# Kernel optimization log

Hardware: AMD Instinct MI355X
Metric: run time of the kernel (lower is better)

Reference implementation:

```python
import math
import jax, jax.numpy as jnp
import numpy as np

B, T, C = 2, 2048, 2048
NQ, NKV, H = 16, 4, 128
EPS = 1e-6
ROPE_BASE = 5.0e6


def setup_inputs() -> dict:
    key = jax.random.key(0)
    ks = jax.random.split(key, 6)
    x = jax.random.normal(ks[0], (B, T, C), dtype=jnp.float32)
    s = 0.02
    Wq = jax.random.normal(ks[1], (C, NQ * H), dtype=jnp.float32) * s
    Wk = jax.random.normal(ks[2], (C, NKV * H), dtype=jnp.float32) * s
    Wv = jax.random.normal(ks[3], (C, NKV * H), dtype=jnp.float32) * s
    Wo = jax.random.normal(ks[4], (NQ * H, C), dtype=jnp.float32) * s
    q_norm_w = jnp.ones((H,), dtype=jnp.float32)
    k_norm_w = jnp.ones((H,), dtype=jnp.float32)
    # RoPE tables (seq_start = 0)
    inv_freq = 1.0 / (ROPE_BASE ** (jnp.arange(0, H, 2, dtype=jnp.float32) / H))
    t = jnp.arange(T, dtype=jnp.float32)
    freqs = jnp.einsum('i,j->ij', t, inv_freq)          # [T, H/2]
    emb = jnp.concatenate([freqs, freqs], axis=-1)       # [T, H]
    cos = jnp.cos(emb)
    sin = jnp.sin(emb)
    # additive causal mask (finite large negative to stay nan-free)
    causal = jnp.tril(jnp.ones((T, T), dtype=bool))
    attn_mask = jnp.where(causal, 0.0, -1e9).astype(jnp.float32)
    return {"x": x, "Wq": Wq, "Wk": Wk, "Wv": Wv, "Wo": Wo,
            "q_norm_w": q_norm_w, "k_norm_w": k_norm_w,
            "cos": cos, "sin": sin, "attn_mask": attn_mask}


def _rms_norm(x, w):
    # x: [..., H]
    var = jnp.mean(x * x, axis=-1, keepdims=True)
    return w * (x * jax.lax.rsqrt(var + EPS))


def _rotate_half(x):
    x1, x2 = jnp.split(x, 2, axis=-1)
    return jnp.concatenate([-x2, x1], axis=-1)


def reference(x, Wq, Wk, Wv, Wo, q_norm_w, k_norm_w, cos, sin, attn_mask):
    q = (x @ Wq).reshape(B, T, NQ, H)
    k = (x @ Wk).reshape(B, T, NKV, H)
    v = (x @ Wv).reshape(B, T, NKV, H)
    q = _rms_norm(q, q_norm_w)
    k = _rms_norm(k, k_norm_w)
    c = cos[None, :, None, :]  # [1,T,1,H]
    s = sin[None, :, None, :]
    q = q * c + _rotate_half(q) * s
    k = k * c + _rotate_half(k) * s
    rep = NQ // NKV
    k = jnp.repeat(k, rep, axis=2)  # [B,T,NQ,H]
    v = jnp.repeat(v, rep, axis=2)
    scores = jnp.einsum('bihd,bjhd->bhij', q, k) / math.sqrt(H)
    scores = scores + attn_mask[None, None, :, :]
    probs = jax.nn.softmax(scores, axis=-1)
    ctx = jnp.einsum('bhij,bjhd->bihd', probs, v).reshape(B, T, NQ * H)
    return ctx @ Wo
```

## Files before the change

kernel.cpp:

```cpp
#include <hip/hip_runtime.h>
#include <hip/hip_bf16.h>

#define B_   2
#define T_   2048
#define C_   2048
#define NQ_  16
#define NKV_ 4
#define H_   128

using bf16x8 = __attribute__((ext_vector_type(8))) short;
using f32x4  = __attribute__((ext_vector_type(4))) float;

__device__ __forceinline__ unsigned short f2bf(float f) {
    __hip_bfloat16 h = __float2bfloat16(f);
    union { __hip_bfloat16 h; unsigned short s; } c;
    c.h = h;
    return c.s;
}
__device__ __forceinline__ float bf2f(unsigned short s) {
    return __uint_as_float(((unsigned)s) << 16);
}
__device__ __forceinline__ bf16x8 pack8(float4 f0, float4 f1) {
    bf16x8 r;
    r[0] = (short)f2bf(f0.x); r[1] = (short)f2bf(f0.y);
    r[2] = (short)f2bf(f0.z); r[3] = (short)f2bf(f0.w);
    r[4] = (short)f2bf(f1.x); r[5] = (short)f2bf(f1.y);
    r[6] = (short)f2bf(f1.z); r[7] = (short)f2bf(f1.w);
    return r;
}

#define MFMA16(a, b, c) __builtin_amdgcn_mfma_f32_16x16x32_bf16(a, b, c, 0, 0, 0)

__global__ void transpose_cvt(const float* __restrict__ src,
                              unsigned short* __restrict__ dst,
                              int R, int Cc) {
    const int tc = Cc >> 6;
    const int r0 = (blockIdx.x / tc) * 64;
    const int c0 = (blockIdx.x % tc) * 64;
    __shared__ unsigned short Tl[64 * 65];
    const int tid = threadIdx.x;
#pragma unroll
    for (int it = 0; it < 16; ++it) {
        const int idx = it * 256 + tid;
        const int r = idx >> 6, c = idx & 63;
        Tl[c * 65 + r] = f2bf(src[(size_t)(r0 + r) * Cc + c0 + c]);
    }
    __syncthreads();
#pragma unroll
    for (int it = 0; it < 16; ++it) {
        const int idx = it * 256 + tid;
        const int c = idx >> 6, r = idx & 63;
        dst[(size_t)(c0 + c) * R + r0 + r] = Tl[c * 65 + r];
    }
}

#define LDP 40

template <bool A_BF, bool OUT_F32>
__global__ __launch_bounds__(256, 2) void gemm_bt(
    const void* __restrict__ Av,
    const unsigned short* __restrict__ Bt,
    void* __restrict__ Cqv,
    unsigned short* __restrict__ Ck,
    unsigned short* __restrict__ Cv,
    int M, int N, int K, int fused) {
    const int ntn = N >> 7;
    const int tm  = blockIdx.x / ntn;
    const int tn  = blockIdx.x % ntn;

    const int tid  = threadIdx.x;
    const int wv   = tid >> 6;
    const int lane = tid & 63;
    const int col  = lane & 15;
    const int quad = lane >> 4;
    const int wm   = (wv & 1) * 64;
    const int wn   = (wv >> 1) * 64;

    __shared__ unsigned short Al[128 * LDP];
    __shared__ unsigned short Bl[128 * LDP];

    f32x4 acc[4][4];
#pragma unroll
    for (int mt = 0; mt < 4; ++mt)
#pragma unroll
        for (int nt = 0; nt < 4; ++nt) acc[mt][nt] = (f32x4){0.f, 0.f, 0.f, 0.f};

    const int i1 = tid, i2 = tid + 256;
    const size_t aoff1 = (size_t)(tm * 128 + (i1 >> 2)) * K + (i1 & 3) * 8;
    const size_t aoff2 = (size_t)(tm * 128 + (i2 >> 2)) * K + (i2 & 3) * 8;
    const size_t boff1 = (size_t)(tn * 128 + (i1 >> 2)) * K + (i1 & 3) * 8;
    const size_t boff2 = (size_t)(tn * 128 + (i2 >> 2)) * K + (i2 & 3) * 8;
    unsigned short* Aw1 = Al + (i1 >> 2) * LDP + (i1 & 3) * 8;
    unsigned short* Aw2 = Al + (i2 >> 2) * LDP + (i2 & 3) * 8;
    unsigned short* Bw1 = Bl + (i1 >> 2) * LDP + (i1 & 3) * 8;
    unsigned short* Bw2 = Bl + (i2 >> 2) * LDP + (i2 & 3) * 8;

    const unsigned short* Ab16 = (const unsigned short*)Av;
    const float*          Af   = (const float*)Av;

    uint4  a1u, a2u, b1u, b2u;
    float4 a1lo, a1hi, a2lo, a2hi;

    auto loadAB = [&](int kk) {
        if constexpr (A_BF) {
            a1u = *(const uint4*)(Ab16 + aoff1 + kk);
            a2u = *(const uint4*)(Ab16 + aoff2 + kk);
        } else {
            a1lo = *(const float4*)(Af + aoff1 + kk);
            a1hi = *(const float4*)(Af + aoff1 + kk + 4);
            a2lo = *(const float4*)(Af + aoff2 + kk);
            a2hi = *(const float4*)(Af + aoff2 + kk + 4);
        }
        b1u = *(const uint4*)(Bt + boff1 + kk);
        b2u = *(const uint4*)(Bt + boff2 + kk);
    };

    loadAB(0);

    for (int k0 = 0; k0 < K; k0 += 32) {
        __syncthreads();
        if constexpr (A_BF) {
            *(uint4*)Aw1 = a1u;
            *(uint4*)Aw2 = a2u;
        } else {
            *(bf16x8*)Aw1 = pack8(a1lo, a1hi);
            *(bf16x8*)Aw2 = pack8(a2lo, a2hi);
        }
        *(uint4*)Bw1 = b1u;
        *(uint4*)Bw2 = b2u;
        __syncthreads();

        const int kn = (k0 + 32 < K) ? k0 + 32 : k0;
        loadAB(kn);

        bf16x8 af[4], bfv[4];
#pragma unroll
        for (int t = 0; t < 4; ++t) {
            af[t]  = *(const bf16x8*)(Al + (wm + t * 16 + col) * LDP + quad * 8);
            bfv[t] = *(const bf16x8*)(Bl + (wn + t * 16 + col) * LDP + quad * 8);
        }
#pragma unroll
        for (int mt = 0; mt < 4; ++mt)
#pragma unroll
            for (int nt = 0; nt < 4; ++nt)
                acc[mt][nt] = MFMA16(af[mt], bfv[nt], acc[mt][nt]);
    }

    const int nb = tn * 128;
    if constexpr (OUT_F32) {
        float* Co = (float*)Cqv;
#pragma unroll
        for (int mt = 0; mt < 4; ++mt)
#pragma unroll
            for (int nt = 0; nt < 4; ++nt)
#pragma unroll
                for (int r = 0; r < 4; ++r) {
                    const int row = tm * 128 + wm + mt * 16 + quad * 4 + r;
                    const int cc  = nb + wn + nt * 16 + col;
                    Co[(size_t)row * N + cc] = acc[mt][nt][r];
                }
    } else {
        unsigned short* Cb;
        int ldc, nc0;
        if (!fused)         { Cb = (unsigned short*)Cqv; ldc = N;    nc0 = nb;        }
        else if (nb < 2048) { Cb = (unsigned short*)Cqv; ldc = 2048; nc0 = nb;        }
        else if (nb < 2560) { Cb = Ck;                   ldc = 512;  nc0 = nb - 2048; }
        else                { Cb = Cv;                   ldc = 512;  nc0 = nb - 2560; }
#pragma unroll
        for (int mt = 0; mt < 4; ++mt)
#pragma unroll
            for (int nt = 0; nt < 4; ++nt)
#pragma unroll
                for (int r = 0; r < 4; ++r) {
                    const int row = tm * 128 + wm + mt * 16 + quad * 4 + r;
                    const int cc  = nc0 + wn + nt * 16 + col;
                    Cb[(size_t)row * ldc + cc] = f2bf(acc[mt][nt][r]);
                }
    }
}

__global__ void norm_rope(unsigned short* __restrict__ buf,
                          const float* __restrict__ w,
                          const float* __restrict__ cosb,
                          const float* __restrict__ sinb,
                          int nheads, float oscale) {
    const int idx = blockIdx.x;
    const int h   = idx % nheads;
    const int bt  = idx / nheads;
    const int t   = bt % T_;
    unsigned short* row = buf + ((size_t)bt * nheads + h) * H_;
    const int l = threadIdx.x;

    const float x0 = bf2f(row[l]);
    const float x1 = bf2f(row[l + 64]);
    float ss = x0 * x0 + x1 * x1;
#pragma unroll
    for (int off = 32; off; off >>= 1) ss += __shfl_xor(ss, off);
    const float r = rsqrtf(ss * (1.0f / 128.0f) + 1e-6f) * oscale;

    const float n0 = x0 * r * w[l];
    const float n1 = x1 * r * w[l + 64];
    const float c0 = cosb[t * H_ + l];
    const float c1 = cosb[t * H_ + l + 64];
    const float s0 = sinb[t * H_ + l];
    const float s1 = sinb[t * H_ + l + 64];

    row[l]      = f2bf(n0 * c0 - n1 * s0);
    row[l + 64] = f2bf(n1 * c1 + n0 * s1);
}

__global__ __launch_bounds__(512, 2) void flash_attn(
    const unsigned short* __restrict__ qbuf,
    const unsigned short* __restrict__ kbuf,
    const unsigned short* __restrict__ vbuf,
    unsigned short* __restrict__ ctx) {
    const int blk = blockIdx.x;
    const int p   = blk & 7;
    const int h   = (blk >> 3) & 15;
    const int b   = blk >> 7;
    const int kvh = h >> 2;
    const int qtB = 15 - p;

    const int tid  = threadIdx.x;
    const int wave = tid >> 6;
    const int g    = wave >> 2;
    const int gw   = wave & 3;
    const int lane = tid & 63;
    const int col  = lane & 15;
    const int quad = lane >> 4;
    const int gtid = gw * 64 + lane;

    int w0 = (g ? qtB : p) * 128 + gw * 32;
    const int ph1 = 2 * p + 2;

    __shared__ __align__(16) unsigned char smem[76800];
    unsigned short* Vg   = (unsigned short*)smem + g * 9216;
    unsigned short* Pw   = (unsigned short*)(smem + 36864) + wave * 2304;
    float*          alfw = (float*)(smem + 73728) + wave * 32;
    unsigned*       Vw   = (unsigned*)Vg;

    bf16x8 qf[2][4];
    auto loadQ = [&]() {
#pragma unroll
        for (int nt = 0; nt < 2; ++nt)
#pragma unroll
            for (int ks = 0; ks < 4; ++ks) {
                const size_t off =
                    ((size_t)(b * T_ + w0 + nt * 16 + col) * NQ_ + h) * H_ + ks * 32 + quad * 8;
                qf[nt][ks] = *(const bf16x8*)(qbuf + off);
            }
    };
    loadQ();

    f32x4 O[2][8];
#pragma unroll
    for (int pt = 0; pt < 2; ++pt)
#pragma unroll
        for (int dt = 0; dt < 8; ++dt) O[pt][dt] = (f32x4){0.f, 0.f, 0.f, 0.f};
    float m_run[2] = {-3.0e38f, -3.0e38f};
    float l_run[2] = {0.f, 0.f};

    bf16x8 kf[4][4];
    const unsigned short* kb = kbuf + ((size_t)(b * T_) * NKV_ + kvh) * H_;
    const int koff = col * (NKV_ * H_) + quad * 8;
    auto loadK = [&](int j0) {
#pragma unroll
        for (int mt = 0; mt < 4; ++mt) {
            const unsigned short* kr = kb + (size_t)((j0 + mt * 16) * (NKV_ * H_) + koff);
#pragma unroll
            for (int ks = 0; ks < 4; ++ks)
                kf[mt][ks] = *(const bf16x8*)(kr + ks * 32);
        }
    };

    uint4 va[4];
    const size_t kvstride = (size_t)NKV_ * H_;
    auto issueV = [&](int j0) {
#pragma unroll
        for (int it = 0; it < 2; ++it) {
            const int idx = it * 256 + gtid;
            const int kp  = idx & 31;
            const int dc  = idx >> 5;
            const size_t g0 = ((size_t)(b * T_ + j0 + 2 * kp) * NKV_ + kvh) * H_ + dc * 8;
            va[2 * it]     = *(const uint4*)(vbuf + g0);
            va[2 * it + 1] = *(const uint4*)(vbuf + g0 + kvstride);
        }
    };
    auto writeV = [&]() {
#pragma unroll
        for (int it = 0; it < 2; ++it) {
            const int idx = it * 256 + gtid;
            const int kp  = idx & 31;
            const int dc  = idx >> 5;
            const uint4 v0 = va[2 * it];
            const uint4 v1 = va[2 * it + 1];
            const int wb = dc * 288 + kp;
            Vw[wb + 0 * 36] = (v0.x & 0xFFFFu) | (v1.x << 16);
            Vw[wb + 1 * 36] = (v0.x >> 16)     | (v1.x & 0xFFFF0000u);
            Vw[wb + 2 * 36] = (v0.y & 0xFFFFu) | (v1.y << 16);
            Vw[wb + 3 * 36] = (v0.y >> 16)     | (v1.y & 0xFFFF0000u);
            Vw[wb + 4 * 36] = (v0.z & 0xFFFFu) | (v1.z << 16);
            Vw[wb + 5 * 36] = (v0.z >> 16)     | (v1.z & 0xFFFF0000u);
            Vw[wb + 6 * 36] = (v0.w & 0xFFFFu) | (v1.w << 16);
            Vw[wb + 7 * 36] = (v0.w >> 16)     | (v1.w & 0xFFFF0000u);
        }
    };

    auto storeOut = [&]() {
        if (quad == 0) {
            alfw[col]      = 1.0f / l_run[0];
            alfw[col + 16] = 1.0f / l_run[1];
        }
        const f32x4 i0 = *(const f32x4*)&alfw[quad * 4];
        const f32x4 i1 = *(const f32x4*)&alfw[quad * 4 + 16];
#pragma unroll
        for (int pt = 0; pt < 2; ++pt)
#pragma unroll
            for (int r = 0; r < 4; ++r) {
                const float inv = pt ? i1[r] : i0[r];
                const int ig = w0 + pt * 16 + quad * 4 + r;
                unsigned short* op = ctx + ((size_t)(b * T_ + ig) * NQ_ + h) * H_;
#pragma unroll
                for (int dt = 0; dt < 8; ++dt)
                    op[dt * 16 + col] = f2bf(O[pt][dt][r] * inv);
            }
    };

    auto chunk_of = [&](int i) { return g ? i : (i < ph1 ? i : i + 15 - 2 * p); };

    loadK(0);
    issueV(0);

    for (int i = 0; i < 17; ++i) {
        const int j0 = chunk_of(i) * 64;
        __syncthreads();
        writeV();
        __syncthreads();

        if (i + 1 < 17) issueV(chunk_of(i + 1) * 64);

        if (g == 0 && i == ph1) {
            storeOut();
#pragma unroll
            for (int pt = 0; pt < 2; ++pt)
#pragma unroll
                for (int dt = 0; dt < 8; ++dt) O[pt][dt] = (f32x4){0.f, 0.f, 0.f, 0.f};
            m_run[0] = m_run[1] = -3.0e38f;
            l_run[0] = l_run[1] = 0.f;
            w0 = qtB * 128 + gw * 32;
            loadQ();
        }

        const bool act = (j0 <= w0 + 31);

        f32x4 St[4][2];
        if (act) {
#pragma unroll
            for (int mt = 0; mt < 4; ++mt)
#pragma unroll
                for (int nt = 0; nt < 2; ++nt) St[mt][nt] = (f32x4){0.f, 0.f, 0.f, 0.f};
#pragma unroll
            for (int ks = 0; ks < 4; ++ks)
#pragma unroll
                for (int mt = 0; mt < 4; ++mt) {
                    St[mt][0] = MFMA16(kf[mt][ks], qf[0][ks], St[mt][0]);
                    St[mt][1] = MFMA16(kf[mt][ks], qf[1][ks], St[mt][1]);
                }
        }

        if (i + 1 < 17) loadK(chunk_of(i + 1) * 64);

        if (!act) continue;

        const bool needmask = (j0 + 63 > w0);
        if (needmask) {
            const int ig0 = w0 + col;
#pragma unroll
            for (int mt = 0; mt < 4; ++mt)
#pragma unroll
                for (int r = 0; r < 4; ++r) {
                    const int key = j0 + mt * 16 + quad * 4 + r;
                    if (key > ig0)      St[mt][0][r] = -3.0e38f;
                    if (key > ig0 + 16) St[mt][1][r] = -3.0e38f;
                }
        }

        float rm[2];
#pragma unroll
        for (int nt = 0; nt < 2; ++nt) {
            float m0 = fmaxf(fmaxf(St[0][nt][0], St[0][nt][1]),
                             fmaxf(St[0][nt][2], St[0][nt][3]));
#pragma unroll
            for (int mt = 1; mt < 4; ++mt)
                m0 = fmaxf(m0, fmaxf(fmaxf(St[mt][nt][0], St[mt][nt][1]),
                                     fmaxf(St[mt][nt][2], St[mt][nt][3])));
            m0 = fmaxf(m0, __shfl_xor(m0, 16));
            m0 = fmaxf(m0, __shfl_xor(m0, 32));
            rm[nt] = m0;
        }

        const int defer = __all((rm[0] <= m_run[0] + 8.0f) && (rm[1] <= m_run[1] + 8.0f));
        if (!defer) {
            const float mn0 = fmaxf(m_run[0], rm[0]);
            const float mn1 = fmaxf(m_run[1], rm[1]);
            const float al0 = exp2f(m_run[0] - mn0);
            const float al1 = exp2f(m_run[1] - mn1);
            m_run[0] = mn0; m_run[1] = mn1;
            l_run[0] *= al0; l_run[1] *= al1;
            if (quad == 0) { alfw[col] = al0; alfw[col + 16] = al1; }
        }

        float ls0 = 0.f, ls1 = 0.f;
#pragma unroll
        for (int mt = 0; mt < 4; ++mt) {
            const float p0 = exp2f(St[mt][0][0] - m_run[0]);
            const float p1 = exp2f(St[mt][0][1] - m_run[0]);
            const float p2 = exp2f(St[mt][0][2] - m_run[0]);
            const float p3 = exp2f(St[mt][0][3] - m_run[0]);
            ls0 += (p0 + p1) + (p2 + p3);
            *(uint2*)(Pw + col * 72 + mt * 16 + quad * 4) =
                make_uint2((unsigned)f2bf(p0) | ((unsigned)f2bf(p1) << 16),
                           (unsigned)f2bf(p2) | ((unsigned)f2bf(p3) << 16));
            const float q0 = exp2f(St[mt][1][0] - m_run[1]);
            const float q1 = exp2f(St[mt][1][1] - m_run[1]);
            const float q2 = exp2f(St[mt][1][2] - m_run[1]);
            const float q3 = exp2f(St[mt][1][3] - m_run[1]);
            ls1 += (q0 + q1) + (q2 + q3);
            *(uint2*)(Pw + (col + 16) * 72 + mt * 16 + quad * 4) =
                make_uint2((unsigned)f2bf(q0) | ((unsigned)f2bf(q1) << 16),
                           (unsigned)f2bf(q2) | ((unsigned)f2bf(q3) << 16));
        }
        ls0 += __shfl_xor(ls0, 16); ls0 += __shfl_xor(ls0, 32);
        ls1 += __shfl_xor(ls1, 16); ls1 += __shfl_xor(ls1, 32);
        l_run[0] += ls0; l_run[1] += ls1;

        if (!defer) {
            const f32x4 a0 = *(const f32x4*)&alfw[quad * 4];
            const f32x4 a1 = *(const f32x4*)&alfw[quad * 4 + 16];
#pragma unroll
            for (int dt = 0; dt < 8; ++dt)
#pragma unroll
                for (int r = 0; r < 4; ++r) { O[0][dt][r] *= a0[r]; O[1][dt][r] *= a1[r]; }
        }

#pragma unroll
        for (int ks = 0; ks < 2; ++ks) {
            const bf16x8 pa0 = *(const bf16x8*)(Pw + col * 72 + ks * 32 + quad * 8);
            const bf16x8 pa1 = *(const bf16x8*)(Pw + (col + 16) * 72 + ks * 32 + quad * 8);
#pragma unroll
            for (int dt = 0; dt < 8; ++dt) {
                const bf16x8 vf = *(const bf16x8*)(Vg + (dt * 16 + col) * 72 + ks * 32 + quad * 8);
                O[0][dt] = MFMA16(pa0, vf, O[0][dt]);
                O[1][dt] = MFMA16(pa1, vf, O[1][dt]);
            }
        }
    }

    __syncthreads();
    float* mlA = (float*)(smem + 74752);
    float* mlB = (float*)(smem + 75776);
    if (g == 0) {
        float* Of = (float*)smem + gw * 4096;
        float* ml = mlA + gw * 64;
        if (quad == 0) {
            ml[2 * col]            = m_run[0]; ml[2 * col + 1]        = l_run[0];
            ml[2 * (col + 16)]     = m_run[1]; ml[2 * (col + 16) + 1] = l_run[1];
        }
#pragma unroll
        for (int pt = 0; pt < 2; ++pt)
#pragma unroll
            for (int dt = 0; dt < 8; ++dt)
#pragma unroll
                for (int r = 0; r < 4; ++r)
                    Of[(pt * 16 + quad * 4 + r) * 128 + dt * 16 + col] = O[pt][dt][r];
    }
    __syncthreads();
    if (g == 1) {
        float* Of = (float*)smem + gw * 4096;
        float* mA = mlA + gw * 64;
        float* mB = mlB + gw * 64;
        if (quad == 0) {
            mB[2 * col]            = m_run[0]; mB[2 * col + 1]        = l_run[0];
            mB[2 * (col + 16)]     = m_run[1]; mB[2 * (col + 16) + 1] = l_run[1];
        }
#pragma unroll
        for (int pt = 0; pt < 2; ++pt)
#pragma unroll
            for (int r = 0; r < 4; ++r) {
                const int row = pt * 16 + quad * 4 + r;
                const float mBv = mB[2 * row], lBv = mB[2 * row + 1];
                const float mAv = mA[2 * row], lAv = mA[2 * row + 1];
                const float m  = fmaxf(mAv, mBv);
                const float aB = exp2f(mBv - m);
                const float aA = exp2f(mAv - m);
                const float inv = 1.0f / (lBv * aB + lAv * aA);
                const int ig = w0 + row;
                unsigned short* op = ctx + ((size_t)(b * T_ + ig) * NQ_ + h) * H_;
#pragma unroll
                for (int dt = 0; dt < 8; ++dt)
                    op[dt * 16 + col] =
                        f2bf((O[pt][dt][r] * aB + Of[row * 128 + dt * 16 + col] * aA) * inv);
            }
    }
}

extern "C" void kernel_launch(void* const* d_in, const int* in_sizes, int n_in,
                              void* d_out, int out_size, void* d_ws, size_t ws_size,
                              hipStream_t stream) {
    const float* x    = (const float*)d_in[0];
    const float* Wq   = (const float*)d_in[1];
    const float* Wk   = (const float*)d_in[2];
    const float* Wv   = (const float*)d_in[3];
    const float* Wo   = (const float*)d_in[4];
    const float* qnw  = (const float*)d_in[5];
    const float* knw  = (const float*)d_in[6];
    const float* cosb = (const float*)d_in[7];
    const float* sinb = (const float*)d_in[8];

    const int M = B_ * T_;
    unsigned short* ws  = (unsigned short*)d_ws;
    unsigned short* WqT = ws;
    unsigned short* WkT = WqT + (size_t)2048 * 2048;
    unsigned short* WvT = WkT + (size_t)512 * 2048;
    unsigned short* ctx = ws;
    unsigned short* q   = ws + (size_t)8388608;
    unsigned short* k   = ws + (size_t)16777216;
    unsigned short* v   = ws + (size_t)18874368;
    unsigned short* WoT = q;

    transpose_cvt<<<(2048 / 64) * (2048 / 64), 256, 0, stream>>>(Wq, WqT, 2048, 2048);
    transpose_cvt<<<(2048 / 64) * (512 / 64),  256, 0, stream>>>(Wk, WkT, 2048, 512);
    transpose_cvt<<<(2048 / 64) * (512 / 64),  256, 0, stream>>>(Wv, WvT, 2048, 512);

    gemm_bt<false, false><<<(M / 128) * (3072 / 128), 256, 0, stream>>>(
        (const void*)x, WqT, (void*)q, k, v, M, 3072, C_, 1);

    norm_rope<<<M * NQ_, 64, 0, stream>>>(q, qnw, cosb, sinb, NQ_, 0.12751743f);
    norm_rope<<<M * NKV_, 64, 0, stream>>>(k, knw, cosb, sinb, NKV_, 1.0f);

    flash_attn<<<256, 512, 0, stream>>>(q, k, v, ctx);

    transpose_cvt<<<(2048 / 64) * (2048 / 64), 256, 0, stream>>>(Wo, WoT, 2048, 2048);
    gemm_bt<true, true><<<(M / 128) * (C_ / 128), 256, 0, stream>>>(
        (const void*)ctx, WoT, d_out, nullptr, nullptr, M, C_, NQ_ * H_, 0);
}
```

Before: 396.4 us.

## Store V transposed from QKV GEMM and load V fragments directly in attention

The QKV GEMM epilogue now writes V tiles transposed into a [b, kvh, d, t] layout, staged through shared memory for coalesced stores. The flash attention kernel then loads V MFMA operands straight from global memory into registers, dropping the per-chunk shared-memory V staging and its two block-wide barriers. This removes the transpose-on-load work and synchronisation from the attention loop. In exchange it raises register pressure (16 extra bf16x8 fragments per thread) and adds an LDS round trip and barriers to the GEMM epilogue for the V tiles.

```diff
diff --git a/kernel.cpp b/kernel.cpp
--- a/kernel.cpp
+++ b/kernel.cpp
@@ -76,8 +76,9 @@
     const int wm   = (wv & 1) * 64;
     const int wn   = (wv >> 1) * 64;
 
-    __shared__ unsigned short Al[128 * LDP];
-    __shared__ unsigned short Bl[128 * LDP];
+    __shared__ unsigned short gsm[17408];
+    unsigned short* Al = gsm;
+    unsigned short* Bl = gsm + 128 * LDP;
 
     f32x4 acc[4][4];
 #pragma unroll
@@ -160,22 +161,46 @@
                     Co[(size_t)row * N + cc] = acc[mt][nt][r];
                 }
     } else {
-        unsigned short* Cb;
-        int ldc, nc0;
-        if (!fused)         { Cb = (unsigned short*)Cqv; ldc = N;    nc0 = nb;        }
-        else if (nb < 2048) { Cb = (unsigned short*)Cqv; ldc = 2048; nc0 = nb;        }
-        else if (nb < 2560) { Cb = Ck;                   ldc = 512;  nc0 = nb - 2048; }
-        else                { Cb = Cv;                   ldc = 512;  nc0 = nb - 2560; }
-#pragma unroll
-        for (int mt = 0; mt < 4; ++mt)
-#pragma unroll
-            for (int nt = 0; nt < 4; ++nt)
-#pragma unroll
-                for (int r = 0; r < 4; ++r) {
-                    const int row = tm * 128 + wm + mt * 16 + quad * 4 + r;
-                    const int cc  = nc0 + wn + nt * 16 + col;
-                    Cb[(size_t)row * ldc + cc] = f2bf(acc[mt][nt][r]);
-                }
+        if (fused && nb >= 2560) {
+            __syncthreads();
+#pragma unroll
+            for (int mt = 0; mt < 4; ++mt)
+#pragma unroll
+                for (int nt = 0; nt < 4; ++nt)
+#pragma unroll
+                    for (int r = 0; r < 4; ++r) {
+                        const int lr = wm + mt * 16 + quad * 4 + r;
+                        const int lc = wn + nt * 16 + col;
+                        gsm[lc * 136 + lr] = f2bf(acc[mt][nt][r]);
+                    }
+            __syncthreads();
+            const int kvh = (nb - 2560) >> 7;
+            const int bb  = tm >> 4;
+            const int t0  = (tm & 15) * 128;
+            unsigned short* dst = Cv + (((size_t)(bb * 4 + kvh)) << 18) + t0;
+#pragma unroll
+            for (int it = 0; it < 8; ++it) {
+                const int d = (tid >> 4) + it * 16;
+                const int t = (tid & 15) * 8;
+                *(uint4*)(dst + (size_t)d * 2048 + t) = *(const uint4*)(gsm + d * 136 + t);
+            }
+        } else {
+            unsigned short* Cb;
+            int ldc, nc0;
+            if (!fused)         { Cb = (unsigned short*)Cqv; ldc = N;    nc0 = nb;        }
+            else if (nb < 2048) { Cb = (unsigned short*)Cqv; ldc = 2048; nc0 = nb;        }
+            else                { Cb = Ck;                   ldc = 512;  nc0 = nb - 2048; }
+#pragma unroll
+            for (int mt = 0; mt < 4; ++mt)
+#pragma unroll
+                for (int nt = 0; nt < 4; ++nt)
+#pragma unroll
+                    for (int r = 0; r < 4; ++r) {
+                        const int row = tm * 128 + wm + mt * 16 + quad * 4 + r;
+                        const int cc  = nc0 + wn + nt * 16 + col;
+                        Cb[(size_t)row * ldc + cc] = f2bf(acc[mt][nt][r]);
+                    }
+        }
     }
 }
 
@@ -212,7 +237,7 @@
 __global__ __launch_bounds__(512, 2) void flash_attn(
     const unsigned short* __restrict__ qbuf,
     const unsigned short* __restrict__ kbuf,
-    const unsigned short* __restrict__ vbuf,
+    const unsigned short* __restrict__ vtg,
     unsigned short* __restrict__ ctx) {
     const int blk = blockIdx.x;
     const int p   = blk & 7;
@@ -228,16 +253,13 @@
     const int lane = tid & 63;
     const int col  = lane & 15;
     const int quad = lane >> 4;
-    const int gtid = gw * 64 + lane;
 
     int w0 = (g ? qtB : p) * 128 + gw * 32;
     const int ph1 = 2 * p + 2;
 
-    __shared__ __align__(16) unsigned char smem[76800];
-    unsigned short* Vg   = (unsigned short*)smem + g * 9216;
-    unsigned short* Pw   = (unsigned short*)(smem + 36864) + wave * 2304;
-    float*          alfw = (float*)(smem + 73728) + wave * 32;
-    unsigned*       Vw   = (unsigned*)Vg;
+    __shared__ __align__(16) unsigned char smem[67584];
+    unsigned short* Pw   = (unsigned short*)smem + wave * 2304;
+    float*          alfw = (float*)(smem + 36864) + wave * 32;
 
     bf16x8 qf[2][4];
     auto loadQ = [&]() {
@@ -273,37 +295,15 @@
         }
     };
 
-    uint4 va[4];
-    const size_t kvstride = (size_t)NKV_ * H_;
-    auto issueV = [&](int j0) {
-#pragma unroll
-        for (int it = 0; it < 2; ++it) {
-            const int idx = it * 256 + gtid;
-            const int kp  = idx & 31;
-            const int dc  = idx >> 5;
-            const size_t g0 = ((size_t)(b * T_ + j0 + 2 * kp) * NKV_ + kvh) * H_ + dc * 8;
-            va[2 * it]     = *(const uint4*)(vbuf + g0);
-            va[2 * it + 1] = *(const uint4*)(vbuf + g0 + kvstride);
-        }
-    };
-    auto writeV = [&]() {
-#pragma unroll
-        for (int it = 0; it < 2; ++it) {
-            const int idx = it * 256 + gtid;
-            const int kp  = idx & 31;
-            const int dc  = idx >> 5;
-            const uint4 v0 = va[2 * it];
-            const uint4 v1 = va[2 * it + 1];
-            const int wb = dc * 288 + kp;
-            Vw[wb + 0 * 36] = (v0.x & 0xFFFFu) | (v1.x << 16);
-            Vw[wb + 1 * 36] = (v0.x >> 16)     | (v1.x & 0xFFFF0000u);
-            Vw[wb + 2 * 36] = (v0.y & 0xFFFFu) | (v1.y << 16);
-            Vw[wb + 3 * 36] = (v0.y >> 16)     | (v1.y & 0xFFFF0000u);
-            Vw[wb + 4 * 36] = (v0.z & 0xFFFFu) | (v1.z << 16);
-            Vw[wb + 5 * 36] = (v0.z >> 16)     | (v1.z & 0xFFFF0000u);
-            Vw[wb + 6 * 36] = (v0.w & 0xFFFFu) | (v1.w << 16);
-            Vw[wb + 7 * 36] = (v0.w >> 16)     | (v1.w & 0xFFFF0000u);
-        }
+    bf16x8 vf[16];
+    const unsigned short* vb =
+        vtg + (((size_t)(b * NKV_ + kvh)) << 18) + col * 2048 + quad * 8;
+    auto loadV = [&](int j0) {
+#pragma unroll
+        for (int dt = 0; dt < 8; ++dt)
+#pragma unroll
+            for (int ks = 0; ks < 2; ++ks)
+                vf[dt * 2 + ks] = *(const bf16x8*)(vb + (size_t)dt * 32768 + j0 + ks * 32);
     };
 
     auto storeOut = [&]() {
@@ -329,15 +329,10 @@
     auto chunk_of = [&](int i) { return g ? i : (i < ph1 ? i : i + 15 - 2 * p); };
 
     loadK(0);
-    issueV(0);
+    loadV(0);
 
     for (int i = 0; i < 17; ++i) {
         const int j0 = chunk_of(i) * 64;
-        __syncthreads();
-        writeV();
-        __syncthreads();
-
-        if (i + 1 < 17) issueV(chunk_of(i + 1) * 64);
 
         if (g == 0 && i == ph1) {
             storeOut();
@@ -366,99 +361,100 @@
                     St[mt][0] = MFMA16(kf[mt][ks], qf[0][ks], St[mt][0]);
                     St[mt][1] = MFMA16(kf[mt][ks], qf[1][ks], St[mt][1]);
                 }
+
+            const bool needmask = (j0 + 63 > w0);
+            if (needmask) {
+                const int ig0 = w0 + col;
+#pragma unroll
+                for (int mt = 0; mt < 4; ++mt)
+#pragma unroll
+                    for (int r = 0; r < 4; ++r) {
+                        const int key = j0 + mt * 16 + quad * 4 + r;
+                        if (key > ig0)      St[mt][0][r] = -3.0e38f;
+                        if (key > ig0 + 16) St[mt][1][r] = -3.0e38f;
+                    }
+            }
+
+            float rm[2];
+#pragma unroll
+            for (int nt = 0; nt < 2; ++nt) {
+                float m0 = fmaxf(fmaxf(St[0][nt][0], St[0][nt][1]),
+                                 fmaxf(St[0][nt][2], St[0][nt][3]));
+#pragma unroll
+                for (int mt = 1; mt < 4; ++mt)
+                    m0 = fmaxf(m0, fmaxf(fmaxf(St[mt][nt][0], St[mt][nt][1]),
+                                         fmaxf(St[mt][nt][2], St[mt][nt][3])));
+                m0 = fmaxf(m0, __shfl_xor(m0, 16));
+                m0 = fmaxf(m0, __shfl_xor(m0, 32));
+                rm[nt] = m0;
+            }
+
+            const int defer = __all((rm[0] <= m_run[0] + 8.0f) && (rm[1] <= m_run[1] + 8.0f));
+            if (!defer) {
+                const float mn0 = fmaxf(m_run[0], rm[0]);
+                const float mn1 = fmaxf(m_run[1], rm[1]);
+                const float al0 = exp2f(m_run[0] - mn0);
+                const float al1 = exp2f(m_run[1] - mn1);
+                m_run[0] = mn0; m_run[1] = mn1;
+                l_run[0] *= al0; l_run[1] *= al1;
+                if (quad == 0) { alfw[col] = al0; alfw[col + 16] = al1; }
+            }
+
+            float ls0 = 0.f, ls1 = 0.f;
+#pragma unroll
+            for (int mt = 0; mt < 4; ++mt) {
+                const float p0 = exp2f(St[mt][0][0] - m_run[0]);
+                const float p1 = exp2f(St[mt][0][1] - m_run[0]);
+                const float p2 = exp2f(St[mt][0][2] - m_run[0]);
+                const float p3 = exp2f(St[mt][0][3] - m_run[0]);
+                ls0 += (p0 + p1) + (p2 + p3);
+                *(uint2*)(Pw + col * 72 + mt * 16 + quad * 4) =
+                    make_uint2((unsigned)f2bf(p0) | ((unsigned)f2bf(p1) << 16),
+                               (unsigned)f2bf(p2) | ((unsigned)f2bf(p3) << 16));
+                const float q0 = exp2f(St[mt][1][0] - m_run[1]);
+                const float q1 = exp2f(St[mt][1][1] - m_run[1]);
+                const float q2 = exp2f(St[mt][1][2] - m_run[1]);
+                const float q3 = exp2f(St[mt][1][3] - m_run[1]);
+                ls1 += (q0 + q1) + (q2 + q3);
+                *(uint2*)(Pw + (col + 16) * 72 + mt * 16 + quad * 4) =
+                    make_uint2((unsigned)f2bf(q0) | ((unsigned)f2bf(q1) << 16),
+                               (unsigned)f2bf(q2) | ((unsigned)f2bf(q3) << 16));
+            }
+            ls0 += __shfl_xor(ls0, 16); ls0 += __shfl_xor(ls0, 32);
+            ls1 += __shfl_xor(ls1, 16); ls1 += __shfl_xor(ls1, 32);
+            l_run[0] += ls0; l_run[1] += ls1;
+
+            if (!defer) {
+                const f32x4 a0 = *(const f32x4*)&alfw[quad * 4];
+                const f32x4 a1 = *(const f32x4*)&alfw[quad * 4 + 16];
+#pragma unroll
+                for (int dt = 0; dt < 8; ++dt)
+#pragma unroll
+                    for (int r = 0; r < 4; ++r) { O[0][dt][r] *= a0[r]; O[1][dt][r] *= a1[r]; }
+            }
         }
 
         if (i + 1 < 17) loadK(chunk_of(i + 1) * 64);
 
-        if (!act) continue;
-
-        const bool needmask = (j0 + 63 > w0);
-        if (needmask) {
-            const int ig0 = w0 + col;
-#pragma unroll
-            for (int mt = 0; mt < 4; ++mt)
-#pragma unroll
-                for (int r = 0; r < 4; ++r) {
-                    const int key = j0 + mt * 16 + quad * 4 + r;
-                    if (key > ig0)      St[mt][0][r] = -3.0e38f;
-                    if (key > ig0 + 16) St[mt][1][r] = -3.0e38f;
+        if (act) {
+#pragma unroll
+            for (int ks = 0; ks < 2; ++ks) {
+                const bf16x8 pa0 = *(const bf16x8*)(Pw + col * 72 + ks * 32 + quad * 8);
+                const bf16x8 pa1 = *(const bf16x8*)(Pw + (col + 16) * 72 + ks * 32 + quad * 8);
+#pragma unroll
+                for (int dt = 0; dt < 8; ++dt) {
+                    O[0][dt] = MFMA16(pa0, vf[dt * 2 + ks], O[0][dt]);
+                    O[1][dt] = MFMA16(pa1, vf[dt * 2 + ks], O[1][dt]);
                 }
-        }
-
-        float rm[2];
-#pragma unroll
-        for (int nt = 0; nt < 2; ++nt) {
-            float m0 = fmaxf(fmaxf(St[0][nt][0], St[0][nt][1]),
-                             fmaxf(St[0][nt][2], St[0][nt][3]));
-#pragma unroll
-            for (int mt = 1; mt < 4; ++mt)
-                m0 = fmaxf(m0, fmaxf(fmaxf(St[mt][nt][0], St[mt][nt][1]),
-                                     fmaxf(St[mt][nt][2], St[mt][nt][3])));
-            m0 = fmaxf(m0, __shfl_xor(m0, 16));
-            m0 = fmaxf(m0, __shfl_xor(m0, 32));
-            rm[nt] = m0;
-        }
-
-        const int defer = __all((rm[0] <= m_run[0] + 8.0f) && (rm[1] <= m_run[1] + 8.0f));
-        if (!defer) {
-            const float mn0 = fmaxf(m_run[0], rm[0]);
-            const float mn1 = fmaxf(m_run[1], rm[1]);
-            const float al0 = exp2f(m_run[0] - mn0);
-            const float al1 = exp2f(m_run[1] - mn1);
-            m_run[0] = mn0; m_run[1] = mn1;
-            l_run[0] *= al0; l_run[1] *= al1;
-            if (quad == 0) { alfw[col] = al0; alfw[col + 16] = al1; }
-        }
-
-        float ls0 = 0.f, ls1 = 0.f;
-#pragma unroll
-        for (int mt = 0; mt < 4; ++mt) {
-            const float p0 = exp2f(St[mt][0][0] - m_run[0]);
-            const float p1 = exp2f(St[mt][0][1] - m_run[0]);
-            const float p2 = exp2f(St[mt][0][2] - m_run[0]);
-            const float p3 = exp2f(St[mt][0][3] - m_run[0]);
-            ls0 += (p0 + p1) + (p2 + p3);
-            *(uint2*)(Pw + col * 72 + mt * 16 + quad * 4) =
-                make_uint2((unsigned)f2bf(p0) | ((unsigned)f2bf(p1) << 16),
-                           (unsigned)f2bf(p2) | ((unsigned)f2bf(p3) << 16));
-            const float q0 = exp2f(St[mt][1][0] - m_run[1]);
-            const float q1 = exp2f(St[mt][1][1] - m_run[1]);
-            const float q2 = exp2f(St[mt][1][2] - m_run[1]);
-            const float q3 = exp2f(St[mt][1][3] - m_run[1]);
-            ls1 += (q0 + q1) + (q2 + q3);
-            *(uint2*)(Pw + (col + 16) * 72 + mt * 16 + quad * 4) =
-                make_uint2((unsigned)f2bf(q0) | ((unsigned)f2bf(q1) << 16),
-                           (unsigned)f2bf(q2) | ((unsigned)f2bf(q3) << 16));
-        }
-        ls0 += __shfl_xor(ls0, 16); ls0 += __shfl_xor(ls0, 32);
-        ls1 += __shfl_xor(ls1, 16); ls1 += __shfl_xor(ls1, 32);
-        l_run[0] += ls0; l_run[1] += ls1;
-
-        if (!defer) {
-            const f32x4 a0 = *(const f32x4*)&alfw[quad * 4];
-            const f32x4 a1 = *(const f32x4*)&alfw[quad * 4 + 16];
-#pragma unroll
-            for (int dt = 0; dt < 8; ++dt)
-#pragma unroll
-                for (int r = 0; r < 4; ++r) { O[0][dt][r] *= a0[r]; O[1][dt][r] *= a1[r]; }
-        }
-
-#pragma unroll
-        for (int ks = 0; ks < 2; ++ks) {
-            const bf16x8 pa0 = *(const bf16x8*)(Pw + col * 72 + ks * 32 + quad * 8);
-            const bf16x8 pa1 = *(const bf16x8*)(Pw + (col + 16) * 72 + ks * 32 + quad * 8);
-#pragma unroll
-            for (int dt = 0; dt < 8; ++dt) {
-                const bf16x8 vf = *(const bf16x8*)(Vg + (dt * 16 + col) * 72 + ks * 32 + quad * 8);
-                O[0][dt] = MFMA16(pa0, vf, O[0][dt]);
-                O[1][dt] = MFMA16(pa1, vf, O[1][dt]);
-            }
-        }
+            }
+        }
+
+        if (i + 1 < 17) loadV(chunk_of(i + 1) * 64);
     }
 
     __syncthreads();
-    float* mlA = (float*)(smem + 74752);
-    float* mlB = (float*)(smem + 75776);
+    float* mlA = (float*)(smem + 65536);
+    float* mlB = (float*)(smem + 66560);
     if (g == 0) {
         float* Of = (float*)smem + gw * 4096;
         float* ml = mlA + gw * 64;
@@ -525,7 +521,7 @@
     unsigned short* ctx = ws;
     unsigned short* q   = ws + (size_t)8388608;
     unsigned short* k   = ws + (size_t)16777216;
-    unsigned short* v   = ws + (size_t)18874368;
+    unsigned short* vtg = ws + (size_t)18874368;
     unsigned short* WoT = q;
 
     transpose_cvt<<<(2048 / 64) * (2048 / 64), 256, 0, stream>>>(Wq, WqT, 2048, 2048);
@@ -533,12 +529,12 @@
     transpose_cvt<<<(2048 / 64) * (512 / 64),  256, 0, stream>>>(Wv, WvT, 2048, 512);
 
     gemm_bt<false, false><<<(M / 128) * (3072 / 128), 256, 0, stream>>>(
-        (const void*)x, WqT, (void*)q, k, v, M, 3072, C_, 1);
+        (const void*)x, WqT, (void*)q, k, vtg, M, 3072, C_, 1);
 
     norm_rope<<<M * NQ_, 64, 0, stream>>>(q, qnw, cosb, sinb, NQ_, 0.12751743f);
     norm_rope<<<M * NKV_, 64, 0, stream>>>(k, knw, cosb, sinb, NKV_, 1.0f);
 
-    flash_attn<<<256, 512, 0, stream>>>(q, k, v, ctx);
+    flash_attn<<<256, 512, 0, stream>>>(q, k, vtg, ctx);
 
     transpose_cvt<<<(2048 / 64) * (2048 / 64), 256, 0, stream>>>(Wo, WoT, 2048, 2048);
     gemm_bt<true, true><<<(M / 128) * (C_ / 128), 256, 0, stream>>>(
```

New measurement: 535.0 us. +35.0%, slower.

## Load GEMM tiles via global_load_lds with XOR swizzle and XCD-aware block remap

Applied to the files above, without the earlier changes.

The GEMM now moves A and B tiles straight from global memory into LDS with global_load_lds, using an XOR-swizzled layout in place of padded rows. A separate kernel first converts x to bf16, writing into the output buffer as scratch, so the QKV GEMM no longer converts fp32 on the fly. Block indices are remapped across the 8 XCDs to improve L2 locality. The register prefetch of the next tile is gone, so global loads are no longer overlapped with MFMA work between the two barriers.

```diff
diff --git a/kernel.cpp b/kernel.cpp
--- a/kernel.cpp
+++ b/kernel.cpp
@@ -30,6 +30,20 @@
 }
 
 #define MFMA16(a, b, c) __builtin_amdgcn_mfma_f32_16x16x32_bf16(a, b, c, 0, 0, 0)
+
+__device__ __forceinline__ void gl_lds16(const void* g, void* l) {
+    __builtin_amdgcn_global_load_lds(
+        (const __attribute__((address_space(1))) void*)g,
+        (__attribute__((address_space(3))) void*)l, 16, 0, 0);
+}
+
+__global__ void cvt_bf16(const float* __restrict__ src,
+                         unsigned short* __restrict__ dst) {
+    const int i = (blockIdx.x * 256 + threadIdx.x) * 8;
+    const float4 a = *(const float4*)(src + i);
+    const float4 b = *(const float4*)(src + i + 4);
+    *(bf16x8*)(dst + i) = pack8(a, b);
+}
 
 __global__ void transpose_cvt(const float* __restrict__ src,
                               unsigned short* __restrict__ dst,
@@ -54,19 +68,19 @@
     }
 }
 
-#define LDP 40
-
-template <bool A_BF, bool OUT_F32>
+template <bool OUT_F32>
 __global__ __launch_bounds__(256, 2) void gemm_bt(
-    const void* __restrict__ Av,
+    const unsigned short* __restrict__ Ab,
     const unsigned short* __restrict__ Bt,
     void* __restrict__ Cqv,
     unsigned short* __restrict__ Ck,
     unsigned short* __restrict__ Cv,
     int M, int N, int K, int fused) {
     const int ntn = N >> 7;
-    const int tm  = blockIdx.x / ntn;
-    const int tn  = blockIdx.x % ntn;
+    const int cpx = gridDim.x >> 3;
+    const int wg  = (blockIdx.x & 7) * cpx + (blockIdx.x >> 3);
+    const int tm  = wg / ntn;
+    const int tn  = wg % ntn;
 
     const int tid  = threadIdx.x;
     const int wv   = tid >> 6;
@@ -76,8 +90,8 @@
     const int wm   = (wv & 1) * 64;
     const int wn   = (wv >> 1) * 64;
 
-    __shared__ unsigned short Al[128 * LDP];
-    __shared__ unsigned short Bl[128 * LDP];
+    __shared__ unsigned short Al[128 * 32];
+    __shared__ unsigned short Bl[128 * 32];
 
     f32x4 acc[4][4];
 #pragma unroll
@@ -85,59 +99,34 @@
 #pragma unroll
         for (int nt = 0; nt < 4; ++nt) acc[mt][nt] = (f32x4){0.f, 0.f, 0.f, 0.f};
 
-    const int i1 = tid, i2 = tid + 256;
-    const size_t aoff1 = (size_t)(tm * 128 + (i1 >> 2)) * K + (i1 & 3) * 8;
-    const size_t aoff2 = (size_t)(tm * 128 + (i2 >> 2)) * K + (i2 & 3) * 8;
-    const size_t boff1 = (size_t)(tn * 128 + (i1 >> 2)) * K + (i1 & 3) * 8;
-    const size_t boff2 = (size_t)(tn * 128 + (i2 >> 2)) * K + (i2 & 3) * 8;
-    unsigned short* Aw1 = Al + (i1 >> 2) * LDP + (i1 & 3) * 8;
-    unsigned short* Aw2 = Al + (i2 >> 2) * LDP + (i2 & 3) * 8;
-    unsigned short* Bw1 = Bl + (i1 >> 2) * LDP + (i1 & 3) * 8;
-    unsigned short* Bw2 = Bl + (i2 >> 2) * LDP + (i2 & 3) * 8;
-
-    const unsigned short* Ab16 = (const unsigned short*)Av;
-    const float*          Af   = (const float*)Av;
-
-    uint4  a1u, a2u, b1u, b2u;
-    float4 a1lo, a1hi, a2lo, a2hi;
-
-    auto loadAB = [&](int kk) {
-        if constexpr (A_BF) {
-            a1u = *(const uint4*)(Ab16 + aoff1 + kk);
-            a2u = *(const uint4*)(Ab16 + aoff2 + kk);
-        } else {
-            a1lo = *(const float4*)(Af + aoff1 + kk);
-            a1hi = *(const float4*)(Af + aoff1 + kk + 4);
-            a2lo = *(const float4*)(Af + aoff2 + kk);
-            a2hi = *(const float4*)(Af + aoff2 + kk + 4);
-        }
-        b1u = *(const uint4*)(Bt + boff1 + kk);
-        b2u = *(const uint4*)(Bt + boff2 + kk);
-    };
-
-    loadAB(0);
+    const int rsl = lane >> 2;
+    const int gsw = ((lane & 3) ^ (rsl & 3)) << 3;
+    const int row0 = wv * 32 + rsl;
+    const int row1 = row0 + 16;
+    const size_t aoff0 = (size_t)(tm * 128 + row0) * K + gsw;
+    const size_t aoff1 = (size_t)(tm * 128 + row1) * K + gsw;
+    const size_t boff0 = (size_t)(tn * 128 + row0) * K + gsw;
+    const size_t boff1 = (size_t)(tn * 128 + row1) * K + gsw;
+    unsigned short* Ad0 = Al + (wv * 32) * 32;
+    unsigned short* Ad1 = Al + (wv * 32 + 16) * 32;
+    unsigned short* Bd0 = Bl + (wv * 32) * 32;
+    unsigned short* Bd1 = Bl + (wv * 32 + 16) * 32;
+
+    const int swq = (quad ^ (col & 3)) << 3;
 
     for (int k0 = 0; k0 < K; k0 += 32) {
         __syncthreads();
-        if constexpr (A_BF) {
-            *(uint4*)Aw1 = a1u;
-            *(uint4*)Aw2 = a2u;
-        } else {
-            *(bf16x8*)Aw1 = pack8(a1lo, a1hi);
-            *(bf16x8*)Aw2 = pack8(a2lo, a2hi);
-        }
-        *(uint4*)Bw1 = b1u;
-        *(uint4*)Bw2 = b2u;
+        gl_lds16(Ab + aoff0 + k0, Ad0);
+        gl_lds16(Ab + aoff1 + k0, Ad1);
+        gl_lds16(Bt + boff0 + k0, Bd0);
+        gl_lds16(Bt + boff1 + k0, Bd1);
         __syncthreads();
 
-        const int kn = (k0 + 32 < K) ? k0 + 32 : k0;
-        loadAB(kn);
-
         bf16x8 af[4], bfv[4];
 #pragma unroll
         for (int t = 0; t < 4; ++t) {
-            af[t]  = *(const bf16x8*)(Al + (wm + t * 16 + col) * LDP + quad * 8);
-            bfv[t] = *(const bf16x8*)(Bl + (wn + t * 16 + col) * LDP + quad * 8);
+            af[t]  = *(const bf16x8*)(Al + (wm + t * 16 + col) * 32 + swq);
+            bfv[t] = *(const bf16x8*)(Bl + (wn + t * 16 + col) * 32 + swq);
         }
 #pragma unroll
         for (int mt = 0; mt < 4; ++mt)
@@ -527,13 +516,15 @@
     unsigned short* k   = ws + (size_t)16777216;
     unsigned short* v   = ws + (size_t)18874368;
     unsigned short* WoT = q;
+    unsigned short* xbf = (unsigned short*)d_out;
 
     transpose_cvt<<<(2048 / 64) * (2048 / 64), 256, 0, stream>>>(Wq, WqT, 2048, 2048);
     transpose_cvt<<<(2048 / 64) * (512 / 64),  256, 0, stream>>>(Wk, WkT, 2048, 512);
     transpose_cvt<<<(2048 / 64) * (512 / 64),  256, 0, stream>>>(Wv, WvT, 2048, 512);
-
-    gemm_bt<false, false><<<(M / 128) * (3072 / 128), 256, 0, stream>>>(
-        (const void*)x, WqT, (void*)q, k, v, M, 3072, C_, 1);
+    cvt_bf16<<<(M * C_) / (256 * 8), 256, 0, stream>>>(x, xbf);
+
+    gemm_bt<false><<<(M / 128) * (3072 / 128), 256, 0, stream>>>(
+        xbf, WqT, (void*)q, k, v, M, 3072, C_, 1);
 
     norm_rope<<<M * NQ_, 64, 0, stream>>>(q, qnw, cosb, sinb, NQ_, 0.12751743f);
     norm_rope<<<M * NKV_, 64, 0, stream>>>(k, knw, cosb, sinb, NKV_, 1.0f);
@@ -541,6 +532,6 @@
     flash_attn<<<256, 512, 0, stream>>>(q, k, v, ctx);
 
     transpose_cvt<<<(2048 / 64) * (2048 / 64), 256, 0, stream>>>(Wo, WoT, 2048, 2048);
-    gemm_bt<true, true><<<(M / 128) * (C_ / 128), 256, 0, stream>>>(
-        (const void*)ctx, WoT, d_out, nullptr, nullptr, M, C_, NQ_ * H_, 0);
-}
+    gemm_bt<true><<<(M / 128) * (C_ / 128), 256, 0, stream>>>(
+        ctx, WoT, d_out, nullptr, nullptr, M, C_, NQ_ * H_, 0);
+}
```

After: 371.3 us. 6.3% less time.
